# Kernel optimization log

Measured on AMD Instinct MI355X. Metric: run time of the kernel, lower is better.

The kernel has to match this reference:

```python
import jax, jax.numpy as jnp
import numpy as np

B, N, C = 32, 8192, 512
K = 128          # fixed number of nonzero rows in column `id` per batch (required for torch.stack)
ID = 37          # column index queried


def setup_inputs() -> dict:
    key = jax.random.key(0)
    k1, k2 = jax.random.split(key)
    # random column per row, avoiding ID
    cols = jax.random.randint(k1, (B, N), 0, C - 1)
    cols = jnp.where(cols >= ID, cols + 1, cols)
    # pick exactly K distinct rows per batch to carry column ID
    perm = jnp.argsort(jax.random.uniform(k2, (B, N)), axis=1)  # [B, N] random row permutation
    sel = perm[:, :K]                                           # [B, K] chosen rows
    batch_idx = jnp.arange(B)[:, None]
    cols = cols.at[batch_idx, sel].set(ID)
    one_hot = jax.nn.one_hot(cols, C, dtype=jnp.float32)        # [B, N, C]
    return {"one_hot": one_hot, "id": ID}


def reference(one_hot, id):
    # zeroing column `id` and subtracting leaves only column `id`; summing over
    # the column dim therefore just extracts one_hot[:, :, id].
    col = one_hot[:, :, id]                       # [B, N]
    block_id = col[:, :, None, None]              # [B, N, 1, 1] == stack(...).unsqueeze(-1)
    # nonzero row indices per batch, ascending, fixed count K (stable sort puts
    # nonzero rows first while preserving ascending row order)
    mask_key = (col == 0).astype(jnp.int32)       # 0 for nonzero rows, 1 otherwise
    indices = jnp.argsort(mask_key, axis=1, stable=True)[:, :K]  # [B, K]
    return block_id, indices
```

## Files before the change

kernel.cpp:

```cpp
#include <hip/hip_runtime.h>

#define PB 32
#define PN 8192
#define PC 512
#define PK 128

typedef float vfloat4 __attribute__((ext_vector_type(4)));


__global__ __launch_bounds__(256) void gather_col(
    const float* __restrict__ one_hot,
    const int* __restrict__ id_ptr,
    float* __restrict__ out0)
{
    const int t    = blockIdx.x * 256 + threadIdx.x;
    const int base = t * 4;
    const int id   = id_ptr[0];

    const float* p = one_hot + (size_t)base * PC + (size_t)id;
    float v0 = __builtin_nontemporal_load(p);
    float v1 = __builtin_nontemporal_load(p + PC);
    float v2 = __builtin_nontemporal_load(p + 2 * PC);
    float v3 = __builtin_nontemporal_load(p + 3 * PC);

    vfloat4 o = { v0, v1, v2, v3 };
    __builtin_nontemporal_store(o, (vfloat4*)(out0 + base));
}

__global__ __launch_bounds__(1024) void compact_idx(
    const float* __restrict__ out0,
    float* __restrict__ out1)
{
    const int b    = blockIdx.x;
    const int tid  = threadIdx.x;
    const int wave = tid >> 6;
    const int lane = tid & 63;

    __shared__ unsigned int wave_cnt[16];

    const float* row = out0 + (size_t)b * PN;

    float vals[8];
#pragma unroll
    for (int p = 0; p < 8; ++p)
        vals[p] = row[p * 1024 + tid];

    unsigned int running = 0;
#pragma unroll
    for (int p = 0; p < 8; ++p) {
        const bool pred = (vals[p] != 0.0f);
        const unsigned long long mask = __ballot(pred);
        if (lane == 0) wave_cnt[wave] = (unsigned int)__popcll(mask);
        __syncthreads();

        unsigned int prefix = 0, total = 0;
#pragma unroll
        for (int w = 0; w < 16; ++w) {
            unsigned int c = wave_cnt[w];
            total += c;
            if (w < wave) prefix += c;
        }

        if (pred) {
            unsigned int rank = (unsigned int)__popcll(mask & ((1ULL << lane) - 1ULL));
            unsigned int pos  = running + prefix + rank;
            if (pos < PK) {
                out1[b * PK + pos] = (float)(p * 1024 + tid);
            }
        }
        running += total;
        __syncthreads();
    }
}

extern "C" void kernel_launch(void* const* d_in, const int* in_sizes, int n_in,
                              void* d_out, int out_size, void* d_ws, size_t ws_size,
                              hipStream_t stream) {
    const float* one_hot = nullptr;
    const int* id_ptr = nullptr;
    for (int i = 0; i < n_in; ++i) {
        if (in_sizes[i] == 1) id_ptr = (const int*)d_in[i];
        else                  one_hot = (const float*)d_in[i];
    }

    float* out0 = (float*)d_out;
    float* out1 = (float*)d_out + (size_t)PB * PN;

    gather_col<<<dim3((PB * PN) / (256 * 4)), dim3(256), 0, stream>>>(one_hot, id_ptr, out0);
    compact_idx<<<dim3(PB), dim3(1024), 0, stream>>>(out0, out1);
}
```

Baseline: 567.7 us.

## Emit ballot bitmasks in gather kernel and compact indices from masks

The gather kernel now uses one thread per row and writes a 64-bit ballot mask per wavefront to workspace. The compaction kernel then reads only these masks, 128 per batch, instead of re-reading the gathered column. It computes offsets with a wave shuffle scan and emits indices by iterating over set bits. This removes the 8-pass ballot/syncthreads loop and the re-read of out0, at the cost of scalar stores instead of vector stores and 4x more blocks in the gather.

```diff
diff --git a/kernel.cpp b/kernel.cpp
--- a/kernel.cpp
+++ b/kernel.cpp
@@ -5,71 +5,55 @@
 #define PC 512
 #define PK 128
 
-typedef float vfloat4 __attribute__((ext_vector_type(4)));
-
 
 __global__ __launch_bounds__(256) void gather_col(
     const float* __restrict__ one_hot,
     const int* __restrict__ id_ptr,
-    float* __restrict__ out0)
+    float* __restrict__ out0,
+    unsigned long long* __restrict__ masks)
 {
-    const int t    = blockIdx.x * 256 + threadIdx.x;
-    const int base = t * 4;
-    const int id   = id_ptr[0];
+    const int t  = blockIdx.x * 256 + threadIdx.x;
+    const int id = id_ptr[0];
 
-    const float* p = one_hot + (size_t)base * PC + (size_t)id;
-    float v0 = __builtin_nontemporal_load(p);
-    float v1 = __builtin_nontemporal_load(p + PC);
-    float v2 = __builtin_nontemporal_load(p + 2 * PC);
-    float v3 = __builtin_nontemporal_load(p + 3 * PC);
+    float v = __builtin_nontemporal_load(one_hot + (size_t)t * PC + (size_t)id);
+    __builtin_nontemporal_store(v, out0 + t);
 
-    vfloat4 o = { v0, v1, v2, v3 };
-    __builtin_nontemporal_store(o, (vfloat4*)(out0 + base));
+    const unsigned long long m = __ballot(v != 0.0f);
+    if ((threadIdx.x & 63) == 0)
+        masks[t >> 6] = m;
 }
 
-__global__ __launch_bounds__(1024) void compact_idx(
-    const float* __restrict__ out0,
+__global__ __launch_bounds__(128) void compact_idx(
+    const unsigned long long* __restrict__ masks,
     float* __restrict__ out1)
 {
     const int b    = blockIdx.x;
     const int tid  = threadIdx.x;
+    const int lane = tid & 63;
     const int wave = tid >> 6;
-    const int lane = tid & 63;
 
-    __shared__ unsigned int wave_cnt[16];
+    __shared__ unsigned int wsum[2];
 
-    const float* row = out0 + (size_t)b * PN;
+    unsigned long long m = masks[b * (PN / 64) + tid];
+    const unsigned int c = (unsigned int)__popcll(m);
 
-    float vals[8];
+    unsigned int inc = c;
 #pragma unroll
-    for (int p = 0; p < 8; ++p)
-        vals[p] = row[p * 1024 + tid];
+    for (int d = 1; d < 64; d <<= 1) {
+        unsigned int up = __shfl_up(inc, d, 64);
+        if (lane >= d) inc += up;
+    }
+    if (lane == 63) wsum[wave] = inc;
+    __syncthreads();
 
-    unsigned int running = 0;
-#pragma unroll
-    for (int p = 0; p < 8; ++p) {
-        const bool pred = (vals[p] != 0.0f);
-        const unsigned long long mask = __ballot(pred);
-        if (lane == 0) wave_cnt[wave] = (unsigned int)__popcll(mask);
-        __syncthreads();
+    unsigned int pos = inc - c + (wave ? wsum[0] : 0u);
 
-        unsigned int prefix = 0, total = 0;
-#pragma unroll
-        for (int w = 0; w < 16; ++w) {
-            unsigned int c = wave_cnt[w];
-            total += c;
-            if (w < wave) prefix += c;
-        }
-
-        if (pred) {
-            unsigned int rank = (unsigned int)__popcll(mask & ((1ULL << lane) - 1ULL));
-            unsigned int pos  = running + prefix + rank;
-            if (pos < PK) {
-                out1[b * PK + pos] = (float)(p * 1024 + tid);
-            }
-        }
-        running += total;
-        __syncthreads();
+    while (m) {
+        const int bit = __builtin_ctzll(m);
+        m &= m - 1;
+        if (pos < PK)
+            out1[b * PK + pos] = (float)(tid * 64 + bit);
+        ++pos;
     }
 }
 
@@ -85,7 +69,9 @@
 
     float* out0 = (float*)d_out;
     float* out1 = (float*)d_out + (size_t)PB * PN;
+    unsigned long long* masks = (unsigned long long*)d_ws;
 
-    gather_col<<<dim3((PB * PN) / (256 * 4)), dim3(256), 0, stream>>>(one_hot, id_ptr, out0);
-    compact_idx<<<dim3(PB), dim3(1024), 0, stream>>>(out0, out1);
+    gather_col<<<dim3((PB * PN) / 256), dim3(256), 0, stream>>>(
+        one_hot, id_ptr, out0, masks);
+    compact_idx<<<dim3(PB), dim3(128), 0, stream>>>(masks, out1);
 }
```

Result: no change. 574.4 us (+1.2%).
